# Performance work log

Hardware: AMD Instinct MI355X
Metric: run time of the kernel (lower is better)

The kernel has to match this reference:

```python
import jax, jax.numpy as jnp
from jax import lax
import numpy as np

B, C, H, W = 4, 256, 128, 128
NC, NH = 19, 8
HD = C // NH
SCALE = HD ** -0.5
MOM = 0.1

def conv2d(x, w, b=None, pad=0, groups=1):
    y = lax.conv_general_dilated(x, w, (1, 1), [(pad, pad), (pad, pad)],
                                 dimension_numbers=('NCHW', 'OIHW', 'NCHW'),
                                 feature_group_count=groups)
    return y if b is None else y + b[None, :, None, None]

def layernorm(x, g, b, eps=1e-5):
    # LN over channel dim (original permutes to NHWC, LN, permutes back)
    mu = x.mean(1, keepdims=True)
    var = jnp.mean((x - mu) ** 2, 1, keepdims=True)
    return (x - mu) / jnp.sqrt(var + eps) * g[None, :, None, None] + b[None, :, None, None]

def setup_inputs():
    key = jax.random.key(0)
    ks = jax.random.split(key, 24)
    s = 0.02
    mem = jax.random.normal(ks[12], (1, NC, C), jnp.float32)
    mem = mem / jnp.linalg.norm(mem, axis=2, keepdims=True)  # F.normalize(dim=2)
    return dict(
        low=jax.random.normal(ks[0], (B, C, H, W), jnp.float32),
        high=jax.random.normal(ks[1], (B, C, H, W), jnp.float32),
        g_low=jnp.ones((C,), jnp.float32), b_low=jnp.zeros((C,), jnp.float32),
        g_high=jnp.ones((C,), jnp.float32), b_high=jnp.zeros((C,), jnp.float32),
        g_mlp=jnp.ones((C,), jnp.float32), b_mlp=jnp.zeros((C,), jnp.float32),
        w_q_dw=jax.random.normal(ks[2], (C, 1, 3, 3), jnp.float32) * s, b_q_dw=jnp.zeros((C,), jnp.float32),
        w_q_pw=jax.random.normal(ks[3], (C, C, 1, 1), jnp.float32) * s, b_q_pw=jnp.zeros((C,), jnp.float32),
        w_ml1=jax.random.normal(ks[4], (C, C // 4, 1, 1), jnp.float32) * s,
        w_ml2=jax.random.normal(ks[5], (NC, C, 1, 1), jnp.float32) * s,
        w_align=jax.random.normal(ks[6], (C, C // 4, 1, 1), jnp.float32) * s,
        w_kv=jax.random.normal(ks[7], (2 * C, C), jnp.float32) * s, b_kv=jnp.zeros((2 * C,), jnp.float32),
        memory=mem,
        w_proj=jax.random.normal(ks[8], (C, C, 1, 1), jnp.float32) * s, b_proj=jnp.zeros((C,), jnp.float32),
        w_mlp1=jax.random.normal(ks[9], (4 * C, C, 1, 1), jnp.float32) * s, b_mlp1=jnp.zeros((4 * C,), jnp.float32),
        w_mlp_dw=jax.random.normal(ks[10], (4 * C, 1, 3, 3), jnp.float32) * s, b_mlp_dw=jnp.zeros((4 * C,), jnp.float32),
        w_mlp2=jax.random.normal(ks[11], (C, 4 * C, 1, 1), jnp.float32) * s, b_mlp2=jnp.zeros((C,), jnp.float32),
    )

def _cpga(low, high, g_low, b_low, g_high, b_high, g_mlp, b_mlp,
          w_q_dw, b_q_dw, w_q_pw, b_q_pw, w_ml1, w_ml2, w_align,
          w_kv, b_kv, memory, w_proj, b_proj,
          w_mlp1, b_mlp1, w_mlp_dw, b_mlp_dw, w_mlp2, b_mlp2):
    query = layernorm(low, g_low, b_low)
    kv_in = layernorm(high, g_high, b_high)
    fused = (query + kv_in) * 0.5
    # CFEmbedding: learned class mask -> spatial softmax -> class prototypes
    mask = conv2d(conv2d(fused, w_ml1, groups=4), w_ml2)           # [B,NC,H,W]
    mask = jax.nn.softmax(mask.reshape(B, NC, H * W), axis=-1)
    xa = conv2d(fused, w_align, groups=4).reshape(B, C, H * W)
    cf = jnp.einsum('bnl,bcl->bnc', mask, xa)                      # [B,NC,C]
    cf = (1.0 - MOM) * cf + MOM * memory                           # memory mix (eval mode)
    kv = jnp.einsum('bnc,dc->bnd', cf, w_kv) + b_kv                # [B,NC,2C]
    k, v = jnp.split(kv, 2, axis=-1)                               # [B,NC,C] each
    # query path: depthwise-separable 3x3 conv
    q = conv2d(query, w_q_dw, b_q_dw, pad=1, groups=C)
    q = conv2d(q, w_q_pw, b_q_pw).reshape(B, NH, HD, H * W)        # [B,NH,HD,HW]
    kh = k.reshape(B, NC, NH, HD)
    vh = v.reshape(B, NC, NH, HD)
    attn = jnp.einsum('bhdl,bnhd->bhln', q, kh) * SCALE            # [B,NH,HW,NC]
    attn = jnp.max(attn, axis=-1, keepdims=True) - attn            # custom max-subtract
    attn = jax.nn.softmax(attn, axis=-1)
    out = jnp.einsum('bhln,bnhd->bhdl', attn, vh).reshape(B, C, H, W)
    out = conv2d(out, w_proj, b_proj) + low                        # residual 1
    # conv FFN: 1x1 expand -> depthwise 3x3 -> GELU -> 1x1 project
    y = layernorm(out, g_mlp, b_mlp)
    y = conv2d(y, w_mlp1, b_mlp1)
    y = conv2d(y, w_mlp_dw, b_mlp_dw, pad=1, groups=4 * C)
    y = jax.nn.gelu(y, approximate=False)
    y = conv2d(y, w_mlp2, b_mlp2)
    return out + y                                                 # residual 2

def reference(low, high, g_low, b_low, g_high, b_high, g_mlp, b_mlp,
              w_q_dw, b_q_dw, w_q_pw, b_q_pw, w_ml1, w_ml2, w_align,
              w_kv, b_kv, memory, w_proj, b_proj,
              w_mlp1, b_mlp1, w_mlp_dw, b_mlp_dw, w_mlp2, b_mlp2):
    return _cpga(low, high, g_low, b_low, g_high, b_high, g_mlp, b_mlp,
                 w_q_dw, b_q_dw, w_q_pw, b_q_pw, w_ml1, w_ml2, w_align,
                 w_kv, b_kv, memory, w_proj, b_proj,
                 w_mlp1, b_mlp1, w_mlp_dw, b_mlp_dw, w_mlp2, b_mlp2)
```

## Files before the change

kernel.cpp:

```cpp
#include <hip/hip_runtime.h>
#include <hip/hip_bf16.h>
#include <math.h>

using bf16 = __hip_bfloat16;
typedef __attribute__((ext_vector_type(8))) short bf16x8s;
typedef __attribute__((ext_vector_type(4))) float f32x4;

#define HWD 16384
#define CD 256
#define BD 4
#define NCD 19
#define SCALE_F 0.17677669529663687f

#define O_GLOW    0
#define O_BLOW    256
#define O_GHIGH   512
#define O_BHIGH   768
#define O_GMLP    1024
#define O_BMLP    1280
#define O_WQDW    1536
#define O_BQDW    3840
#define O_WQPW    4096
#define O_BQPW    69632
#define O_WML1    69888
#define O_WML2    86272
#define O_WALIGN  91136
#define O_WKV     107520
#define O_BKV     238592
#define O_MEM     239104
#define O_WPROJ   243968
#define O_BPROJ   309504
#define O_WMLP1   309760
#define O_BMLP1   571904
#define O_WMLPDW  572928
#define O_BMLPDW  582144
#define O_WMLP2   583168
#define O_BMLP2   845312
#define WTOTAL    845568

__device__ __forceinline__ float bfv(const bf16* p){ return __bfloat162float(*p); }
__device__ __forceinline__ float ldi(const void* p, size_t i, bool f32){
  return f32 ? ((const float*)p)[i] : __bfloat162float(((const bf16*)p)[i]);
}
__device__ __forceinline__ void sto(void* p, size_t i, float v, bool f32){
  if (f32) ((float*)p)[i] = v; else ((bf16*)p)[i] = __float2bfloat16(v);
}

__global__ void detect_kernel(const unsigned* __restrict__ g, int* __restrict__ flag){
  if (threadIdx.x == 0) *flag = (g[0] == 0x3F800000u) ? 1 : 0;
}

struct WSrc { const void* p[24]; };
__global__ __launch_bounds__(256) void convert_kernel(WSrc a, bf16* __restrict__ WB,
                                                      const int* __restrict__ flag){
  const bool fin = *flag != 0;
  const int SZ[24] = {256,256,256,256,256,256, 2304,256, 65536,256,
                      16384,4864,16384, 131072,512,4864, 65536,256,
                      262144,1024, 9216,1024, 262144,256};
  size_t i = (size_t)blockIdx.x*256 + threadIdx.x;
  if (i >= WTOTAL) return;
  size_t base = 0; int seg = 0; size_t loc = 0;
  #pragma unroll
  for (int s = 0; s < 24; s++){
    if (i >= base && i < base + (size_t)SZ[s]){ seg = s; loc = i - base; }
    base += (size_t)SZ[s];
  }
  WB[i] = __float2bfloat16(ldi(a.p[seg], loc, fin));
}

__global__ __launch_bounds__(256) void ln_fuse_kernel(
    const void* __restrict__ low, const void* __restrict__ high,
    const bf16* __restrict__ WB, bf16* __restrict__ Q, bf16* __restrict__ F,
    const int* __restrict__ flag){
  const bool fin = *flag != 0;
  __shared__ float red[4][64][4];
  __shared__ float stats[4][64];
  int t = threadIdx.x;
  int px = t & 63, cs = t >> 6;
  int lg0 = blockIdx.x * 64;
  int b = lg0 >> 14, ll0 = lg0 & (HWD-1);
  size_t base = (size_t)b*CD*HWD + (size_t)ll0 + px;
  int c0 = cs*64;
  float s1=0.f,s2=0.f,u1=0.f,u2=0.f;
  for (int k=0;k<64;k++){
    float xl = ldi(low,  base + (size_t)(c0+k)*HWD, fin);
    float xh = ldi(high, base + (size_t)(c0+k)*HWD, fin);
    s1+=xl; s2+=xl*xl; u1+=xh; u2+=xh*xh;
  }
  red[cs][px][0]=s1; red[cs][px][1]=s2; red[cs][px][2]=u1; red[cs][px][3]=u2;
  __syncthreads();
  if (cs==0){
    float a=0.f,bb=0.f,c=0.f,d=0.f;
    #pragma unroll
    for (int j=0;j<4;j++){ a+=red[j][px][0]; bb+=red[j][px][1]; c+=red[j][px][2]; d+=red[j][px][3]; }
    float ml=a*(1.f/CD), vl=bb*(1.f/CD)-ml*ml;
    float mh=c*(1.f/CD), vh=d*(1.f/CD)-mh*mh;
    stats[0][px]=ml; stats[1][px]=rsqrtf(vl+1e-5f);
    stats[2][px]=mh; stats[3][px]=rsqrtf(vh+1e-5f);
  }
  __syncthreads();
  float ml=stats[0][px], rl=stats[1][px], mh=stats[2][px], rh=stats[3][px];
  bf16* qr = Q + (size_t)(lg0+px)*CD + c0;
  bf16* fr = F + (size_t)(lg0+px)*CD + c0;
  for (int k8=0;k8<8;k8++){
    uint4 qo, fo;
    bf16* qp=(bf16*)&qo; bf16* fp=(bf16*)&fo;
    #pragma unroll
    for (int i=0;i<8;i++){
      int c = c0 + k8*8 + i;
      float xl = ldi(low,  base + (size_t)c*HWD, fin);
      float xh = ldi(high, base + (size_t)c*HWD, fin);
      float q = (xl-ml)*rl*bfv(WB+O_GLOW+c) + bfv(WB+O_BLOW+c);
      float h = (xh-mh)*rh*bfv(WB+O_GHIGH+c) + bfv(WB+O_BHIGH+c);
      qp[i] = __float2bfloat16(q);
      fp[i] = __float2bfloat16(0.5f*(q+h));
    }
    *(uint4*)(qr + k8*8) = qo;
    *(uint4*)(fr + k8*8) = fo;
  }
}

__global__ __launch_bounds__(256) void ln_kernel(
    const bf16* __restrict__ x, const bf16* __restrict__ WB, bf16* __restrict__ out){
  int lg = blockIdx.x*256 + threadIdx.x;
  const bf16* xr = x + (size_t)lg*CD;
  float s1=0.f, s2=0.f;
  for (int v8=0; v8<32; v8++){
    uint4 vv = *(const uint4*)(xr + v8*8);
    const bf16* bb = (const bf16*)&vv;
    #pragma unroll
    for (int i=0;i<8;i++){ float x0 = __bfloat162float(bb[i]); s1+=x0; s2+=x0*x0; }
  }
  float m = s1*(1.f/CD), v = s2*(1.f/CD)-m*m, r = rsqrtf(v+1e-5f);
  bf16* orr = out + (size_t)lg*CD;
  for (int v8=0; v8<32; v8++){
    uint4 vv = *(const uint4*)(xr + v8*8);
    const bf16* bb = (const bf16*)&vv;
    #pragma unroll
    for (int i=0;i<8;i++){
      int c = v8*8+i;
      orr[c] = __float2bfloat16((__bfloat162float(bb[i])-m)*r*bfv(WB+O_GMLP+c) + bfv(WB+O_BMLP+c));
    }
  }
}

template<int K, bool GROUPED, int OUTMODE, int RESMODE, bool HASBIAS, bool SWAP>
__global__ __launch_bounds__(256) void gemm_kernel(
    const bf16* __restrict__ X, int xstride,
    const bf16* __restrict__ W, const bf16* __restrict__ bias,
    const void* __restrict__ resv, void* __restrict__ outv,
    int ostride, int co_limit, int out_off, const int* __restrict__ flag){
  __shared__ bf16 As[64*32];
  __shared__ bf16 Bs[256*32];
  int t = threadIdx.x, w = t>>6, lane = t&63;
  int l0 = blockIdx.x*256;
  int co0 = blockIdx.y*64;
  int koff = GROUPED ? co0 : 0;
  f32x4 acc[4][4];
  #pragma unroll
  for (int i=0;i<4;i++)
    #pragma unroll
    for (int j=0;j<4;j++) acc[i][j] = (f32x4){0.f,0.f,0.f,0.f};

  int a_row = t>>2, a_k8 = (t&3)*8;
  int a_co = co0 + a_row; if (a_co >= co_limit) a_co = co_limit-1;
  const bf16* aW = W + (size_t)a_co*K + a_k8;
  const bf16* bX = X + (size_t)(l0 + t)*xstride + koff;
  bf16* asw = As + t*8;
  bf16* bsw = Bs + t*32;
  int frow = lane & 15, fk = (lane>>4)*8;
  const bf16* xrd = Bs + ((w*64 + frow)*32 + fk);
  const bf16* wrd = As + (frow*32 + fk);

  for (int k0 = 0; k0 < K; k0 += 32){
    uint4 av  = *(const uint4*)(aW + k0);
    uint4 bv0 = *(const uint4*)(bX + k0);
    uint4 bv1 = *(const uint4*)(bX + k0 + 8);
    uint4 bv2 = *(const uint4*)(bX + k0 + 16);
    uint4 bv3 = *(const uint4*)(bX + k0 + 24);
    __syncthreads();
    *(uint4*)asw = av;
    *(uint4*)(bsw)    = bv0;  *(uint4*)(bsw+8)  = bv1;
    *(uint4*)(bsw+16) = bv2;  *(uint4*)(bsw+24) = bv3;
    __syncthreads();
    bf16x8s xf[4], wf[4];
    #pragma unroll
    for (int i=0;i<4;i++){
      xf[i] = *(const bf16x8s*)(xrd + i*512);
      wf[i] = *(const bf16x8s*)(wrd + i*512);
    }
    #pragma unroll
    for (int i=0;i<4;i++)
      #pragma unroll
      for (int j=0;j<4;j++)
        acc[i][j] = SWAP
          ? __builtin_amdgcn_mfma_f32_16x16x32_bf16(wf[i], xf[j], acc[i][j], 0,0,0)
          : __builtin_amdgcn_mfma_f32_16x16x32_bf16(xf[i], wf[j], acc[i][j], 0,0,0);
  }

  const bool fio = *flag != 0;
  #pragma unroll
  for (int i=0;i<4;i++){
    #pragma unroll
    for (int j=0;j<4;j++){
      #pragma unroll
      for (int r=0;r<4;r++){
        int l, co;
        if (SWAP){ co = co0 + i*16 + (lane>>4)*4 + r; l = l0 + w*64 + j*16 + (lane&15); }
        else     { l = l0 + w*64 + i*16 + (lane>>4)*4 + r; co = co0 + j*16 + (lane&15); }
        float v = acc[i][j][r];
        if (HASBIAS) v += __bfloat162float(bias[co]);
        if (RESMODE==2){
          int b = l>>14, ll = l & (HWD-1);
          v += ldi(resv, ((size_t)(b*CD+co))*HWD + ll, fio);
        }
        if (RESMODE==1) v += __bfloat162float(((const bf16*)resv)[(size_t)l*CD + co]);
        if (OUTMODE==0) ((bf16*)outv)[(size_t)l*ostride + co] = __float2bfloat16(v);
        else if (OUTMODE==1){ if (co < co_limit) ((float*)outv)[(size_t)l*ostride + co] = v; }
        else sto(outv, (size_t)out_off + (size_t)co*HWD + l, v, fio);
      }
    }
  }
}

template<int CH, bool GELU>
__global__ __launch_bounds__(256) void dw3x3_kernel(
    const bf16* __restrict__ x, const bf16* __restrict__ w,
    const bf16* __restrict__ bias, bf16* __restrict__ out){
  constexpr int CPG = CH/8;
  constexpr int PPI = 256/CPG;
  constexpr int PPB = PPI*8;
  int t = threadIdx.x;
  int cg = t % CPG, pr = t / CPG;
  int c0 = cg*8;
  float wv[8][9], bv[8];
  #pragma unroll
  for (int i=0;i<8;i++){
    bv[i] = __bfloat162float(bias[c0+i]);
    #pragma unroll
    for (int k=0;k<9;k++) wv[i][k] = __bfloat162float(w[(c0+i)*9+k]);
  }
  int p0 = blockIdx.x * PPB;
  for (int it=0; it<8; it++){
    int px = p0 + it*PPI + pr;
    int l = px & (HWD-1);
    int y = l >> 7, xx = l & 127;
    float acc[8];
    #pragma unroll
    for (int i=0;i<8;i++) acc[i] = bv[i];
    #pragma unroll
    for (int dy=-1;dy<=1;dy++){
      int yy = y+dy; if ((unsigned)yy >= 128u) continue;
      #pragma unroll
      for (int dx=-1;dx<=1;dx++){
        int x2 = xx+dx; if ((unsigned)x2 >= 128u) continue;
        const bf16* pp = x + ((size_t)px + dy*128 + dx)*CH + c0;
        uint4 vv = *(const uint4*)pp;
        const bf16* bb = (const bf16*)&vv;
        float wk0 = wv[0][(dy+1)*3+dx+1];
        #pragma unroll
        for (int i=0;i<8;i++) acc[i] += wv[i][(dy+1)*3+dx+1]*__bfloat162float(bb[i]);
        (void)wk0;
      }
    }
    bf16* orow = out + (size_t)px*CH + c0;
    #pragma unroll
    for (int i=0;i<8;i++){
      float v = acc[i];
      if (GELU) v = 0.5f*v*(1.f+erff(v*0.70710678118f));
      orow[i] = __float2bfloat16(v);
    }
  }
}

__global__ __launch_bounds__(256) void pmax_kernel(const float* __restrict__ M, float* __restrict__ PMX){
  int b = blockIdx.y, tile = blockIdx.x, t = threadIdx.x;
  float mx[NCD];
  #pragma unroll
  for (int n=0;n<NCD;n++) mx[n] = -1e30f;
  for (int p = t; p < 512; p += 256){
    const float* r = M + ((size_t)b*HWD + tile*512 + p)*NCD;
    #pragma unroll
    for (int n=0;n<NCD;n++) mx[n] = fmaxf(mx[n], r[n]);
  }
  int lane = t&63, wv = t>>6;
  __shared__ float red[4][NCD];
  #pragma unroll
  for (int n=0;n<NCD;n++){
    float v = mx[n];
    for (int o=32;o;o>>=1) v = fmaxf(v, __shfl_down(v,o));
    if (lane==0) red[wv][n] = v;
  }
  __syncthreads();
  if (t < NCD)
    PMX[(b*32+tile)*NCD + t] = fmaxf(fmaxf(red[0][t],red[1][t]), fmaxf(red[2][t],red[3][t]));
}

__global__ void fmax_kernel(const float* __restrict__ PMX, float* __restrict__ MX, float* __restrict__ DEN){
  int t = threadIdx.x;
  if (t < BD*NCD){
    int b = t / NCD, n = t % NCD;
    float v = -1e30f;
    for (int i=0;i<32;i++) v = fmaxf(v, PMX[(b*32+i)*NCD + n]);
    MX[t] = v; DEN[t] = 0.f;
  }
}

__global__ __launch_bounds__(256) void exp_kernel(float* __restrict__ M,
    const float* __restrict__ MX, float* __restrict__ DEN){
  int b = blockIdx.y, t = threadIdx.x;
  float* r = M + ((size_t)b*HWD + blockIdx.x*256 + t)*NCD;
  float den[NCD];
  #pragma unroll
  for (int n=0;n<NCD;n++){ float e = expf(r[n] - MX[b*NCD+n]); r[n] = e; den[n] = e; }
  int lane = t&63, wv = t>>6;
  __shared__ float red[4][NCD];
  #pragma unroll
  for (int n=0;n<NCD;n++){
    float v = den[n];
    for (int o=32;o;o>>=1) v += __shfl_down(v,o);
    if (lane==0) red[wv][n] = v;
  }
  __syncthreads();
  if (t < NCD) atomicAdd(&DEN[b*NCD+t], red[0][t]+red[1][t]+red[2][t]+red[3][t]);
}

__global__ __launch_bounds__(256) void cfp_kernel(const float* __restrict__ M,
    const bf16* __restrict__ xa, float* __restrict__ PCF){
  int b = blockIdx.y, lt = blockIdx.x, c = threadIdx.x;
  float acc[NCD];
  #pragma unroll
  for (int n=0;n<NCD;n++) acc[n] = 0.f;
  for (int p=0;p<256;p++){
    size_t l = (size_t)b*HWD + lt*256 + p;
    float xv = __bfloat162float(xa[l*CD + c]);
    const float* e = M + l*NCD;
    #pragma unroll
    for (int n=0;n<NCD;n++) acc[n] += e[n]*xv;
  }
  float* o = PCF + ((size_t)(b*64+lt)*NCD)*CD + c;
  #pragma unroll
  for (int n=0;n<NCD;n++) o[n*CD] = acc[n];
}

__global__ __launch_bounds__(256) void cfr_kernel(const float* __restrict__ PCF,
    const float* __restrict__ DEN, float* __restrict__ CF){
  int idx = blockIdx.x*256 + threadIdx.x;
  if (idx >= BD*NCD*CD) return;
  int c = idx & 255, bn = idx >> 8;
  int b = bn / NCD, n = bn % NCD;
  float s = 0.f;
  for (int lt=0; lt<64; lt++) s += PCF[((size_t)(b*64+lt)*NCD + n)*CD + c];
  CF[(size_t)bn*CD + c] = s / DEN[b*NCD+n];
}

__global__ __launch_bounds__(256) void kv_kernel(const float* __restrict__ CF,
    const bf16* __restrict__ WB, float* __restrict__ KV){
  int idx = blockIdx.x*256 + threadIdx.x;
  if (idx >= BD*NCD*512) return;
  int d = idx & 511, bn = idx >> 9;
  int n = bn % NCD;
  float acc = bfv(WB + O_BKV + d);
  const float* cfr = CF + (size_t)bn*CD;
  const bf16* mr = WB + O_MEM + n*CD;
  const bf16* wr = WB + O_WKV + (size_t)d*CD;
  for (int c=0;c<CD;c++)
    acc += (0.9f*cfr[c] + 0.1f*bfv(mr+c)) * bfv(wr+c);
  KV[(size_t)bn*512 + d] = acc;
}

__global__ __launch_bounds__(256) void attn_kernel(const bf16* __restrict__ q,
    const float* __restrict__ KV, bf16* __restrict__ out){
  __shared__ float ks[NCD][256], vs[NCD][256];
  int t = threadIdx.x;
  int b = blockIdx.y, lt = blockIdx.x;
  for (int i=t; i<NCD*512; i+=256){
    int n = i>>9, d = i&511;
    float v = KV[(size_t)(b*NCD+n)*512 + d];
    if (d < 256) ks[n][d] = v; else vs[n][d-256] = v;
  }
  __syncthreads();
  int p = t & 31, h = t >> 5;
  size_t lg = (size_t)b*HWD + lt*32 + p;
  const bf16* qr = q + lg*CD + h*32;
  float qd[32];
  #pragma unroll
  for (int v8=0; v8<4; v8++){
    uint4 vv = *(const uint4*)(qr + v8*8);
    const bf16* bb = (const bf16*)&vv;
    #pragma unroll
    for (int i=0;i<8;i++) qd[v8*8+i] = __bfloat162float(bb[i]);
  }
  float s[NCD];
  #pragma unroll
  for (int n=0;n<NCD;n++){
    const float* kr = &ks[n][h*32];
    float a = 0.f;
    #pragma unroll
    for (int d=0;d<32;d++) a += qd[d]*kr[d];
    s[n] = a * SCALE_F;
  }
  float mn = s[0];
  #pragma unroll
  for (int n=1;n<NCD;n++) mn = fminf(mn, s[n]);
  float sum = 0.f;
  #pragma unroll
  for (int n=0;n<NCD;n++){ s[n] = expf(mn - s[n]); sum += s[n]; }
  float inv = 1.f/sum;
  bf16* orow = out + lg*CD + h*32;
  #pragma unroll
  for (int d=0;d<32;d++){
    float o = 0.f;
    #pragma unroll
    for (int n=0;n<NCD;n++) o += s[n]*vs[n][h*32+d];
    orow[d] = __float2bfloat16(o*inv);
  }
}

extern "C" void kernel_launch(void* const* d_in, const int* in_sizes, int n_in,
                              void* d_out, int out_size, void* d_ws, size_t ws_size,
                              hipStream_t stream){
  const void* low  = d_in[0];
  const void* high = d_in[1];

  char* ws = (char*)d_ws;
  bf16* B1 = (bf16*)(ws);
  bf16* B2 = (bf16*)(ws + ((size_t)32<<20));
  bf16* B3 = (bf16*)(ws + ((size_t)64<<20));
  bf16* B4 = (bf16*)(ws + ((size_t)96<<20));
  float* M  = (float*)(ws + ((size_t)128<<20));
  float* PCF= (float*)(ws + ((size_t)134<<20));
  bf16* WB  = (bf16*)(ws + ((size_t)140<<20));
  float* PMX= (float*)(ws + ((size_t)142<<20));
  float* MX = (float*)(ws + ((size_t)142<<20) + (64<<10));
  float* DEN= (float*)(ws + ((size_t)142<<20) + (80<<10));
  float* CF = (float*)(ws + ((size_t)142<<20) + (96<<10));
  float* KV = (float*)(ws + ((size_t)142<<20) + (256<<10));
  int* FLAG = (int*)  (ws + ((size_t)142<<20) + (512<<10));

  dim3 blk(256);

  detect_kernel<<<1, 64, 0, stream>>>((const unsigned*)d_in[2], FLAG);

  WSrc src;
  for (int i=0;i<24;i++) src.p[i] = d_in[i+2];
  convert_kernel<<<(WTOTAL+255)/256, blk, 0, stream>>>(src, WB, FLAG);

  ln_fuse_kernel<<<1024, blk, 0, stream>>>(low, high, WB, B1, B2, FLAG);
  gemm_kernel<64,true,0,0,false,false><<<dim3(256,4), blk, 0, stream>>>(
      B2, 256, WB+O_WML1, nullptr, nullptr, B3, 256, 256, 0, FLAG);
  gemm_kernel<256,false,1,0,false,false><<<dim3(256,1), blk, 0, stream>>>(
      B3, 256, WB+O_WML2, nullptr, nullptr, M, NCD, NCD, 0, FLAG);
  pmax_kernel<<<dim3(32,BD), blk, 0, stream>>>(M, PMX);
  fmax_kernel<<<1, 128, 0, stream>>>(PMX, MX, DEN);
  exp_kernel<<<dim3(64,BD), blk, 0, stream>>>(M, MX, DEN);
  gemm_kernel<64,true,0,0,false,false><<<dim3(256,4), blk, 0, stream>>>(
      B2, 256, WB+O_WALIGN, nullptr, nullptr, B3, 256, 256, 0, FLAG);
  cfp_kernel<<<dim3(64,BD), blk, 0, stream>>>(M, B3, PCF);
  cfr_kernel<<<(BD*NCD*CD+255)/256, blk, 0, stream>>>(PCF, DEN, CF);
  kv_kernel<<<(BD*NCD*512+255)/256, blk, 0, stream>>>(CF, WB, KV);
  dw3x3_kernel<256,false><<<1024, blk, 0, stream>>>(B1, WB+O_WQDW, WB+O_BQDW, B2);
  gemm_kernel<256,false,0,0,true,false><<<dim3(256,4), blk, 0, stream>>>(
      B2, 256, WB+O_WQPW, WB+O_BQPW, nullptr, B3, 256, 256, 0, FLAG);
  attn_kernel<<<dim3(512,BD), blk, 0, stream>>>(B3, KV, B2);
  gemm_kernel<256,false,0,2,true,false><<<dim3(256,4), blk, 0, stream>>>(
      B2, 256, WB+O_WPROJ, WB+O_BPROJ, low, B1, 256, 256, 0, FLAG);
  ln_kernel<<<256, blk, 0, stream>>>(B1, WB, B2);
  for (int b = 0; b < BD; b++){
    gemm_kernel<256,false,0,0,true,false><<<dim3(64,16), blk, 0, stream>>>(
        B2 + (size_t)b*HWD*CD, 256, WB+O_WMLP1, WB+O_BMLP1, nullptr, B3, 1024, 1024, 0, FLAG);
    dw3x3_kernel<1024,true><<<1024, blk, 0, stream>>>(B3, WB+O_WMLPDW, WB+O_BMLPDW, B4);
    gemm_kernel<1024,false,2,1,true,true><<<dim3(64,4), blk, 0, stream>>>(
        B4, 1024, WB+O_WMLP2, WB+O_BMLP2, B1 + (size_t)b*HWD*CD, d_out, 0, 256, b*CD*HWD, FLAG);
  }
}
```

Baseline: 1.117 ms.

## Vectorize LayerNorm-fuse loads with LDS-staged stores; use direct global-to-LDS loads in GEMM

The fused LayerNorm kernel now has each thread read four contiguous pixels per channel with float4 or ushort4 loads. Q and F are built through a shared-memory tile so the channel-last outputs go out as coalesced 16-byte stores, where before each thread wrote its own scattered rows. The GEMM now fills its LDS tiles with global_load_lds instead of loading into registers and writing to shared memory. In exchange, the inputs are read three times instead of twice, and the GEMM must rely on the builtin's lane-to-LDS layout matching the fragment reads, with no explicit wait on those asynchronous loads before the barrier.

```diff
diff --git a/kernel.cpp b/kernel.cpp
--- a/kernel.cpp
+++ b/kernel.cpp
@@ -46,6 +46,12 @@
   if (f32) ((float*)p)[i] = v; else ((bf16*)p)[i] = __float2bfloat16(v);
 }
 
+__device__ __forceinline__ void gld16(const bf16* g, bf16* l){
+  __builtin_amdgcn_global_load_lds(
+      (const __attribute__((address_space(1))) unsigned int*)g,
+      (__attribute__((address_space(3))) unsigned int*)l, 16, 0, 0);
+}
+
 __global__ void detect_kernel(const unsigned* __restrict__ g, int* __restrict__ flag){
   if (threadIdx.x == 0) *flag = (g[0] == 0x3F800000u) ? 1 : 0;
 }
@@ -73,50 +79,124 @@
     const bf16* __restrict__ WB, bf16* __restrict__ Q, bf16* __restrict__ F,
     const int* __restrict__ flag){
   const bool fin = *flag != 0;
-  __shared__ float red[4][64][4];
+  union SMU { float red[16][64][4]; bf16 tile[64][256]; };
+  __shared__ SMU sm;
   __shared__ float stats[4][64];
   int t = threadIdx.x;
-  int px = t & 63, cs = t >> 6;
+  int pq = t & 15, cs = t >> 4;
   int lg0 = blockIdx.x * 64;
   int b = lg0 >> 14, ll0 = lg0 & (HWD-1);
-  size_t base = (size_t)b*CD*HWD + (size_t)ll0 + px;
-  int c0 = cs*64;
-  float s1=0.f,s2=0.f,u1=0.f,u2=0.f;
-  for (int k=0;k<64;k++){
-    float xl = ldi(low,  base + (size_t)(c0+k)*HWD, fin);
-    float xh = ldi(high, base + (size_t)(c0+k)*HWD, fin);
-    s1+=xl; s2+=xl*xl; u1+=xh; u2+=xh*xh;
-  }
-  red[cs][px][0]=s1; red[cs][px][1]=s2; red[cs][px][2]=u1; red[cs][px][3]=u2;
-  __syncthreads();
-  if (cs==0){
-    float a=0.f,bb=0.f,c=0.f,d=0.f;
-    #pragma unroll
-    for (int j=0;j<4;j++){ a+=red[j][px][0]; bb+=red[j][px][1]; c+=red[j][px][2]; d+=red[j][px][3]; }
-    float ml=a*(1.f/CD), vl=bb*(1.f/CD)-ml*ml;
+  size_t pbase = (size_t)b*CD*HWD + (size_t)ll0 + pq*4;
+  int c0 = cs*16;
+
+  float s1[4]={0,0,0,0}, s2[4]={0,0,0,0}, u1[4]={0,0,0,0}, u2[4]={0,0,0,0};
+  for (int k=0;k<16;k++){
+    size_t off = pbase + (size_t)(c0+k)*HWD;
+    float xl[4], xh[4];
+    if (fin){
+      float4 a = *(const float4*)((const float*)low + off);
+      float4 h = *(const float4*)((const float*)high + off);
+      xl[0]=a.x; xl[1]=a.y; xl[2]=a.z; xl[3]=a.w;
+      xh[0]=h.x; xh[1]=h.y; xh[2]=h.z; xh[3]=h.w;
+    } else {
+      ushort4 a = *(const ushort4*)((const bf16*)low + off);
+      ushort4 h = *(const ushort4*)((const bf16*)high + off);
+      const bf16* ap=(const bf16*)&a; const bf16* hp=(const bf16*)&h;
+      #pragma unroll
+      for (int q=0;q<4;q++){ xl[q]=__bfloat162float(ap[q]); xh[q]=__bfloat162float(hp[q]); }
+    }
+    #pragma unroll
+    for (int q=0;q<4;q++){
+      s1[q]+=xl[q]; s2[q]+=xl[q]*xl[q];
+      u1[q]+=xh[q]; u2[q]+=xh[q]*xh[q];
+    }
+  }
+  #pragma unroll
+  for (int q=0;q<4;q++){
+    sm.red[cs][pq*4+q][0]=s1[q]; sm.red[cs][pq*4+q][1]=s2[q];
+    sm.red[cs][pq*4+q][2]=u1[q]; sm.red[cs][pq*4+q][3]=u2[q];
+  }
+  __syncthreads();
+  if (t < 64){
+    float a=0.f,b2=0.f,c=0.f,d=0.f;
+    #pragma unroll
+    for (int j=0;j<16;j++){
+      a+=sm.red[j][t][0]; b2+=sm.red[j][t][1];
+      c+=sm.red[j][t][2]; d+=sm.red[j][t][3];
+    }
+    float ml=a*(1.f/CD), vl=b2*(1.f/CD)-ml*ml;
     float mh=c*(1.f/CD), vh=d*(1.f/CD)-mh*mh;
-    stats[0][px]=ml; stats[1][px]=rsqrtf(vl+1e-5f);
-    stats[2][px]=mh; stats[3][px]=rsqrtf(vh+1e-5f);
-  }
-  __syncthreads();
-  float ml=stats[0][px], rl=stats[1][px], mh=stats[2][px], rh=stats[3][px];
-  bf16* qr = Q + (size_t)(lg0+px)*CD + c0;
-  bf16* fr = F + (size_t)(lg0+px)*CD + c0;
-  for (int k8=0;k8<8;k8++){
-    uint4 qo, fo;
-    bf16* qp=(bf16*)&qo; bf16* fp=(bf16*)&fo;
-    #pragma unroll
-    for (int i=0;i<8;i++){
-      int c = c0 + k8*8 + i;
-      float xl = ldi(low,  base + (size_t)c*HWD, fin);
-      float xh = ldi(high, base + (size_t)c*HWD, fin);
-      float q = (xl-ml)*rl*bfv(WB+O_GLOW+c) + bfv(WB+O_BLOW+c);
-      float h = (xh-mh)*rh*bfv(WB+O_GHIGH+c) + bfv(WB+O_BHIGH+c);
-      qp[i] = __float2bfloat16(q);
-      fp[i] = __float2bfloat16(0.5f*(q+h));
-    }
-    *(uint4*)(qr + k8*8) = qo;
-    *(uint4*)(fr + k8*8) = fo;
+    stats[0][t]=ml; stats[1][t]=rsqrtf(vl+1e-5f);
+    stats[2][t]=mh; stats[3][t]=rsqrtf(vh+1e-5f);
+  }
+  __syncthreads();
+  float mlq[4],rlq[4],mhq[4],rhq[4];
+  #pragma unroll
+  for (int q=0;q<4;q++){
+    mlq[q]=stats[0][pq*4+q]; rlq[q]=stats[1][pq*4+q];
+    mhq[q]=stats[2][pq*4+q]; rhq[q]=stats[3][pq*4+q];
+  }
+
+  for (int k=0;k<16;k++){
+    int c = c0+k;
+    size_t off = pbase + (size_t)c*HWD;
+    float xl[4];
+    if (fin){
+      float4 a = *(const float4*)((const float*)low + off);
+      xl[0]=a.x; xl[1]=a.y; xl[2]=a.z; xl[3]=a.w;
+    } else {
+      ushort4 a = *(const ushort4*)((const bf16*)low + off);
+      const bf16* ap=(const bf16*)&a;
+      #pragma unroll
+      for (int q=0;q<4;q++) xl[q]=__bfloat162float(ap[q]);
+    }
+    float g = bfv(WB+O_GLOW+c), bb = bfv(WB+O_BLOW+c);
+    #pragma unroll
+    for (int q=0;q<4;q++)
+      sm.tile[pq*4+q][c] = __float2bfloat16((xl[q]-mlq[q])*rlq[q]*g + bb);
+  }
+  __syncthreads();
+  {
+    bf16* qb = Q + (size_t)lg0*CD;
+    const uint4* src = (const uint4*)&sm.tile[0][0];
+    #pragma unroll
+    for (int it=0; it<8; it++)
+      *(uint4*)(qb + ((size_t)it*256 + t)*8) = src[it*256 + t];
+  }
+  __syncthreads();
+
+  for (int k=0;k<16;k++){
+    int c = c0+k;
+    size_t off = pbase + (size_t)c*HWD;
+    float xl[4], xh[4];
+    if (fin){
+      float4 a = *(const float4*)((const float*)low + off);
+      float4 h = *(const float4*)((const float*)high + off);
+      xl[0]=a.x; xl[1]=a.y; xl[2]=a.z; xl[3]=a.w;
+      xh[0]=h.x; xh[1]=h.y; xh[2]=h.z; xh[3]=h.w;
+    } else {
+      ushort4 a = *(const ushort4*)((const bf16*)low + off);
+      ushort4 h = *(const ushort4*)((const bf16*)high + off);
+      const bf16* ap=(const bf16*)&a; const bf16* hp=(const bf16*)&h;
+      #pragma unroll
+      for (int q=0;q<4;q++){ xl[q]=__bfloat162float(ap[q]); xh[q]=__bfloat162float(hp[q]); }
+    }
+    float gl = bfv(WB+O_GLOW+c),  bl = bfv(WB+O_BLOW+c);
+    float gh = bfv(WB+O_GHIGH+c), bh = bfv(WB+O_BHIGH+c);
+    #pragma unroll
+    for (int q=0;q<4;q++){
+      float qv = (xl[q]-mlq[q])*rlq[q]*gl + bl;
+      float hv = (xh[q]-mhq[q])*rhq[q]*gh + bh;
+      sm.tile[pq*4+q][c] = __float2bfloat16(0.5f*(qv+hv));
+    }
+  }
+  __syncthreads();
+  {
+    bf16* fb = F + (size_t)lg0*CD;
+    const uint4* src = (const uint4*)&sm.tile[0][0];
+    #pragma unroll
+    for (int it=0; it<8; it++)
+      *(uint4*)(fb + ((size_t)it*256 + t)*8) = src[it*256 + t];
   }
 }
 
@@ -162,26 +242,21 @@
     #pragma unroll
     for (int j=0;j<4;j++) acc[i][j] = (f32x4){0.f,0.f,0.f,0.f};
 
-  int a_row = t>>2, a_k8 = (t&3)*8;
-  int a_co = co0 + a_row; if (a_co >= co_limit) a_co = co_limit-1;
-  const bf16* aW = W + (size_t)a_co*K + a_k8;
-  const bf16* bX = X + (size_t)(l0 + t)*xstride + koff;
-  bf16* asw = As + t*8;
-  bf16* bsw = Bs + t*32;
+  int sub = lane>>2, kp = lane&3;
+  int a_co = co0 + w*16 + sub; if (a_co >= co_limit) a_co = co_limit-1;
+  const bf16* aW = W + (size_t)a_co*K + kp*8;
+  const bf16* bRow = X + (size_t)(l0 + w*64 + sub)*xstride + koff + kp*8;
+  bf16* aL = As + w*512;
   int frow = lane & 15, fk = (lane>>4)*8;
   const bf16* xrd = Bs + ((w*64 + frow)*32 + fk);
   const bf16* wrd = As + (frow*32 + fk);
 
   for (int k0 = 0; k0 < K; k0 += 32){
-    uint4 av  = *(const uint4*)(aW + k0);
-    uint4 bv0 = *(const uint4*)(bX + k0);
-    uint4 bv1 = *(const uint4*)(bX + k0 + 8);
-    uint4 bv2 = *(const uint4*)(bX + k0 + 16);
-    uint4 bv3 = *(const uint4*)(bX + k0 + 24);
     __syncthreads();
-    *(uint4*)asw = av;
-    *(uint4*)(bsw)    = bv0;  *(uint4*)(bsw+8)  = bv1;
-    *(uint4*)(bsw+16) = bv2;  *(uint4*)(bsw+24) = bv3;
+    gld16(aW + k0, aL);
+    #pragma unroll
+    for (int j=0;j<4;j++)
+      gld16(bRow + (size_t)j*16*xstride + k0, Bs + (size_t)(w*4+j)*512);
     __syncthreads();
     bf16x8s xf[4], wf[4];
     #pragma unroll
@@ -257,10 +332,8 @@
         const bf16* pp = x + ((size_t)px + dy*128 + dx)*CH + c0;
         uint4 vv = *(const uint4*)pp;
         const bf16* bb = (const bf16*)&vv;
-        float wk0 = wv[0][(dy+1)*3+dx+1];
         #pragma unroll
         for (int i=0;i<8;i++) acc[i] += wv[i][(dy+1)*3+dx+1]*__bfloat162float(bb[i]);
-        (void)wk0;
       }
     }
     bf16* orow = out + (size_t)px*CH + c0;
```

Result: faster. 945.7 us (-15.3%).
